# Kernel optimization log

Measured on AMD Instinct MI355X. Metric: run time of the kernel, lower is better.

The kernel has to match this reference:

```python
import jax, jax.numpy as jnp
import numpy as np

STREAMS = 4
SINKHORN_ITERS = 10
SINKHORN_TAU = 0.05


def sinkhorn_log(logits, num_iters=SINKHORN_ITERS, tau=SINKHORN_TAU):
    n = logits.shape[-1]
    Z = logits / tau
    log_marginal = -jnp.log(jnp.asarray(n, logits.dtype))

    def step(carry, _):
        u, v = carry
        u = log_marginal - jax.nn.logsumexp(Z + v[None, :], axis=1)
        v = log_marginal - jax.nn.logsumexp(Z + u[:, None], axis=0)
        return (u, v), None

    u0 = jnp.zeros((n,), logits.dtype)
    v0 = jnp.zeros((n,), logits.dtype)
    (u, v), _ = jax.lax.scan(step, (u0, v0), None, length=num_iters)
    return jnp.exp(Z + u[:, None] + v[None, :]) * n


def setup_inputs() -> dict:
    key = jax.random.key(0)
    k1, = jax.random.split(key, 1)
    B, S, T, D = 2, STREAMS, 4096, 2048
    residuals = jax.random.normal(k1, (B * S, T, D), dtype=jnp.float32)
    # __init__ initialization (layer_index = 0)
    H_res_logits = jnp.full((S, S), -8.0, dtype=jnp.float32)
    H_res_logits = H_res_logits.at[jnp.arange(S), jnp.arange(S)].set(0.0)
    H_pre_logits = jnp.full((S,), -8.0, dtype=jnp.float32).at[0].set(0.0)
    H_post_logits = jnp.zeros((S,), dtype=jnp.float32)
    return {
        "residuals": residuals,
        "H_res_logits": H_res_logits,
        "H_pre_logits": H_pre_logits,
        "H_post_logits": H_post_logits,
    }


def reference(residuals, H_res_logits, H_pre_logits, H_post_logits):
    BS, T, D = residuals.shape
    S = STREAMS
    B = BS // S
    # (b s) t d -> b t s d   (streams are the inner factor of the batch dim)
    x = residuals.reshape(B, S, T, D).transpose(0, 2, 1, 3)

    H_res = sinkhorn_log(H_res_logits)                 # [s, s] doubly-stochastic * n
    H_pre = jax.nn.softmax(H_pre_logits, axis=-1)      # [s]
    H_post = jax.nn.softmax(H_post_logits, axis=-1)    # [s]

    # width connection: mix residual streams, reduce to branch input
    residuals_mixed = jnp.einsum("st,blsd->bltd", H_res, x)   # b t s d
    branch_input = jnp.einsum("s,blsd->bld", H_pre, x)        # b t d

    # branch = Identity (branch=None in __init__)
    branch_output = branch_input

    # depth connection: residuals_mixed + H_post (x) branch_output
    out = residuals_mixed + H_post[None, None, :, None] * branch_output[:, :, None, :]

    # b t s d -> (b s) t d
    return out.transpose(0, 2, 1, 3).reshape(BS, T, D)
```

## Files before the change

### kernel.cpp

```cpp
#include <hip/hip_runtime.h>
#include <math.h>

#define NS 4
#define SINKHORN_ITERS 10
#define TAU 0.05f

#define PLANE4 2097152L
#define PLANE4_SHIFT 21
#define NTHREADS (1 << 20)

typedef float f32x4 __attribute__((ext_vector_type(4)));

__global__ void hc_coef_kernel(const float* __restrict__ Hres_logits,
                               const float* __restrict__ Hpre_logits,
                               const float* __restrict__ Hpost_logits,
                               float* __restrict__ M) {
    if (threadIdx.x != 0 || blockIdx.x != 0) return;

    float Z[NS][NS], u[NS], v[NS];
    for (int i = 0; i < NS; ++i)
        for (int j = 0; j < NS; ++j)
            Z[i][j] = Hres_logits[i * NS + j] / TAU;

    const float logm = -logf((float)NS);
    for (int i = 0; i < NS; ++i) { u[i] = 0.f; v[i] = 0.f; }

    for (int it = 0; it < SINKHORN_ITERS; ++it) {
        for (int i = 0; i < NS; ++i) {
            float mx = -INFINITY;
            for (int j = 0; j < NS; ++j) mx = fmaxf(mx, Z[i][j] + v[j]);
            float s = 0.f;
            for (int j = 0; j < NS; ++j) s += expf(Z[i][j] + v[j] - mx);
            u[i] = logm - (mx + logf(s));
        }
        for (int j = 0; j < NS; ++j) {
            float mx = -INFINITY;
            for (int i = 0; i < NS; ++i) mx = fmaxf(mx, Z[i][j] + u[i]);
            float s = 0.f;
            for (int i = 0; i < NS; ++i) s += expf(Z[i][j] + u[i] - mx);
            v[j] = logm - (mx + logf(s));
        }
    }

    float Hres[NS][NS];
    for (int i = 0; i < NS; ++i)
        for (int j = 0; j < NS; ++j)
            Hres[i][j] = expf(Z[i][j] + u[i] + v[j]) * (float)NS;

    float hp[NS], mx = -INFINITY, s = 0.f;
    for (int i = 0; i < NS; ++i) mx = fmaxf(mx, Hpre_logits[i]);
    for (int i = 0; i < NS; ++i) { hp[i] = expf(Hpre_logits[i] - mx); s += hp[i]; }
    for (int i = 0; i < NS; ++i) hp[i] /= s;

    float ho[NS];
    mx = -INFINITY; s = 0.f;
    for (int i = 0; i < NS; ++i) mx = fmaxf(mx, Hpost_logits[i]);
    for (int i = 0; i < NS; ++i) { ho[i] = expf(Hpost_logits[i] - mx); s += ho[i]; }
    for (int i = 0; i < NS; ++i) ho[i] /= s;

    for (int so = 0; so < NS; ++so)
        for (int si = 0; si < NS; ++si)
            M[so * NS + si] = Hres[si][so] + ho[so] * hp[si];
}

__global__ __launch_bounds__(256) void hc_mix_flat(
        const f32x4* __restrict__ in,
        const float* __restrict__ Mg,
        f32x4* __restrict__ out) {
    float m[16];
#pragma unroll
    for (int k = 0; k < 16; ++k) m[k] = Mg[k];

    const long bb   = blockIdx.x >> 11;
    const long q    = ((long)(blockIdx.x & 2047) << 10) + threadIdx.x;
    const long base = bb * (NS * PLANE4) + q;

    f32x4 v[4][NS];
#pragma unroll
    for (int k = 0; k < 4; ++k)
#pragma unroll
        for (int s = 0; s < NS; ++s)
            v[k][s] = in[base + (long)s * PLANE4 + k * 256];

#pragma unroll
    for (int k = 0; k < 4; ++k)
#pragma unroll
        for (int o = 0; o < NS; ++o) {
            f32x4 r = m[o*4+0] * v[k][0] + m[o*4+1] * v[k][1] +
                      m[o*4+2] * v[k][2] + m[o*4+3] * v[k][3];
            __builtin_nontemporal_store(r, &out[base + (long)o * PLANE4 + k * 256]);
        }
}

__global__ __launch_bounds__(256) void hc_mix_generic(
        const f32x4* __restrict__ in,
        const float* __restrict__ Mg,
        f32x4* __restrict__ out,
        int npos4) {
    float m[16];
#pragma unroll
    for (int k = 0; k < 16; ++k) m[k] = Mg[k];

    const int stride = gridDim.x * blockDim.x;
    for (int p = blockIdx.x * blockDim.x + threadIdx.x; p < npos4; p += stride) {
        const int b = p >> PLANE4_SHIFT;
        const long base = ((long)(b * NS) << PLANE4_SHIFT) + (p & (PLANE4 - 1));
        const f32x4 v0 = in[base];
        const f32x4 v1 = in[base + PLANE4];
        const f32x4 v2 = in[base + 2 * PLANE4];
        const f32x4 v3 = in[base + 3 * PLANE4];
#pragma unroll
        for (int o = 0; o < NS; ++o) {
            f32x4 r = m[o*4+0]*v0 + m[o*4+1]*v1 + m[o*4+2]*v2 + m[o*4+3]*v3;
            __builtin_nontemporal_store(r, &out[base + (long)o * PLANE4]);
        }
    }
}

extern "C" void kernel_launch(void* const* d_in, const int* in_sizes, int n_in,
                              void* d_out, int out_size, void* d_ws, size_t ws_size,
                              hipStream_t stream) {
    const float* residuals   = (const float*)d_in[0];
    const float* Hres_logits = (const float*)d_in[1];
    const float* Hpre_logits = (const float*)d_in[2];
    const float* Hpost_logits= (const float*)d_in[3];
    float* out = (float*)d_out;
    float* M   = (float*)d_ws;

    hc_coef_kernel<<<1, 64, 0, stream>>>(Hres_logits, Hpre_logits, Hpost_logits, M);

    const int npos4 = out_size / (NS * 4);
    if (npos4 == 4 * NTHREADS) {
        hc_mix_flat<<<NTHREADS / 256, 256, 0, stream>>>(
            (const f32x4*)residuals, M, (f32x4*)out);
    } else {
        hc_mix_generic<<<2048, 256, 0, stream>>>(
            (const f32x4*)residuals, M, (f32x4*)out, npos4);
    }
}
```

Baseline: 101.0 us.

## Fuse Sinkhorn coefficient computation into the mixing kernel per block

Drops the separate single-thread coefficient kernel launch on the fast path. Each block now has thread 0 compute the 4x4 mixing matrix redundantly into shared memory after the residual loads are issued, followed by a block barrier. This removes one launch and the dependency gap between kernels, but adds serial Sinkhorn work (exp/log loops) to every one of the 4096 blocks and a __syncthreads that stalls the other threads while thread 0 computes.

Measured after the change: 120.4 us. 19.2% more time.

```diff
diff --git a/kernel.cpp b/kernel.cpp
--- a/kernel.cpp
+++ b/kernel.cpp
@@ -11,12 +11,10 @@
 
 typedef float f32x4 __attribute__((ext_vector_type(4)));
 
-__global__ void hc_coef_kernel(const float* __restrict__ Hres_logits,
-                               const float* __restrict__ Hpre_logits,
-                               const float* __restrict__ Hpost_logits,
-                               float* __restrict__ M) {
-    if (threadIdx.x != 0 || blockIdx.x != 0) return;
-
+__device__ void compute_M_serial(const float* __restrict__ Hres_logits,
+                                 const float* __restrict__ Hpre_logits,
+                                 const float* __restrict__ Hpost_logits,
+                                 float* __restrict__ m ) {
     float Z[NS][NS], u[NS], v[NS];
     for (int i = 0; i < NS; ++i)
         for (int j = 0; j < NS; ++j)
@@ -42,11 +40,6 @@
         }
     }
 
-    float Hres[NS][NS];
-    for (int i = 0; i < NS; ++i)
-        for (int j = 0; j < NS; ++j)
-            Hres[i][j] = expf(Z[i][j] + u[i] + v[j]) * (float)NS;
-
     float hp[NS], mx = -INFINITY, s = 0.f;
     for (int i = 0; i < NS; ++i) mx = fmaxf(mx, Hpre_logits[i]);
     for (int i = 0; i < NS; ++i) { hp[i] = expf(Hpre_logits[i] - mx); s += hp[i]; }
@@ -60,16 +53,17 @@
 
     for (int so = 0; so < NS; ++so)
         for (int si = 0; si < NS; ++si)
-            M[so * NS + si] = Hres[si][so] + ho[so] * hp[si];
+            m[so * NS + si] = expf(Z[si][so] + u[si] + v[so]) * (float)NS
+                              + ho[so] * hp[si];
 }
 
-__global__ __launch_bounds__(256) void hc_mix_flat(
+__global__ __launch_bounds__(256) void hc_fused(
         const f32x4* __restrict__ in,
-        const float* __restrict__ Mg,
+        const float* __restrict__ Hres_logits,
+        const float* __restrict__ Hpre_logits,
+        const float* __restrict__ Hpost_logits,
         f32x4* __restrict__ out) {
-    float m[16];
-#pragma unroll
-    for (int k = 0; k < 16; ++k) m[k] = Mg[k];
+    __shared__ float Msh[16];
 
     const long bb   = blockIdx.x >> 11;
     const long q    = ((long)(blockIdx.x & 2047) << 10) + threadIdx.x;
@@ -82,6 +76,17 @@
         for (int s = 0; s < NS; ++s)
             v[k][s] = in[base + (long)s * PLANE4 + k * 256];
 
+    if (threadIdx.x == 0) {
+        float m[16];
+        compute_M_serial(Hres_logits, Hpre_logits, Hpost_logits, m);
+        for (int k = 0; k < 16; ++k) Msh[k] = m[k];
+    }
+    __syncthreads();
+
+    float m[16];
+#pragma unroll
+    for (int k = 0; k < 16; ++k) m[k] = Msh[k];
+
 #pragma unroll
     for (int k = 0; k < 4; ++k)
 #pragma unroll
@@ -90,6 +95,16 @@
                       m[o*4+2] * v[k][2] + m[o*4+3] * v[k][3];
             __builtin_nontemporal_store(r, &out[base + (long)o * PLANE4 + k * 256]);
         }
+}
+
+__global__ void hc_coef_kernel(const float* __restrict__ Hres_logits,
+                               const float* __restrict__ Hpre_logits,
+                               const float* __restrict__ Hpost_logits,
+                               float* __restrict__ M) {
+    if (threadIdx.x != 0 || blockIdx.x != 0) return;
+    float m[16];
+    compute_M_serial(Hres_logits, Hpre_logits, Hpost_logits, m);
+    for (int k = 0; k < 16; ++k) M[k] = m[k];
 }
 
 __global__ __launch_bounds__(256) void hc_mix_generic(
@@ -127,13 +142,13 @@
     float* out = (float*)d_out;
     float* M   = (float*)d_ws;
 
-    hc_coef_kernel<<<1, 64, 0, stream>>>(Hres_logits, Hpre_logits, Hpost_logits, M);
-
     const int npos4 = out_size / (NS * 4);
     if (npos4 == 4 * NTHREADS) {
-        hc_mix_flat<<<NTHREADS / 256, 256, 0, stream>>>(
-            (const f32x4*)residuals, M, (f32x4*)out);
+        hc_fused<<<NTHREADS / 256, 256, 0, stream>>>(
+            (const f32x4*)residuals, Hres_logits, Hpre_logits, Hpost_logits,
+            (f32x4*)out);
     } else {
+        hc_coef_kernel<<<1, 64, 0, stream>>>(Hres_logits, Hpre_logits, Hpost_logits, M);
         hc_mix_generic<<<2048, 256, 0, stream>>>(
             (const f32x4*)residuals, M, (f32x4*)out, npos4);
     }
```
